# Optimization experiments

Measured on AMD Instinct MI355X. Metric: run time of the kernel, lower is better.

## Reference

```python
import jax, jax.numpy as jnp
import numpy as np

N = 50000      # num_nodes
NT = 300000    # unique (s, o) pairs
R = 64         # num relations
RP = 16        # latent pseudo-relations
E = 32         # emb_dim
C = 32         # num_classes
LW = 64        # latent MLP width


def setup_inputs() -> dict:
    key = jax.random.key(0)
    ks = jax.random.split(key, 12)
    inp = {
        "s_idx": jax.random.randint(ks[0], (NT,), 0, N, dtype=jnp.int32),
        "o_idx": jax.random.randint(ks[1], (NT,), 0, N, dtype=jnp.int32),
        "nhots": jax.random.uniform(ks[2], (NT, R), dtype=jnp.float32),
        "W1a": jax.random.normal(ks[3], (R, LW), dtype=jnp.float32) * 0.1,
        "b1a": jnp.zeros((LW,), jnp.float32),
        "W1b": jax.random.normal(ks[4], (LW, RP), dtype=jnp.float32) * 0.1,
        "b1b": jnp.zeros((RP,), jnp.float32),
        "W2a": jax.random.normal(ks[5], (R, LW), dtype=jnp.float32) * 0.1,
        "b2a": jnp.zeros((LW,), jnp.float32),
        "W2b": jax.random.normal(ks[6], (LW, RP), dtype=jnp.float32) * 0.1,
        "b2b": jnp.zeros((RP,), jnp.float32),
        "weights1": jax.random.normal(ks[7], (RP, N, E), dtype=jnp.float32) * 0.05,
        "weights2": jax.random.normal(ks[8], (RP, E, C), dtype=jnp.float32) * 0.05,
        "bias1": jnp.zeros((E,), jnp.float32),
        "bias2": jnp.zeros((C,), jnp.float32),
    }
    return inp


def _mlp(x, Wa, ba, Wb, bb):
    # Linear(r, lwidth) -> ReLU -> Linear(lwidth, rp)
    return jax.nn.relu(x @ Wa + ba) @ Wb + bb


def reference(s_idx, o_idx, nhots, W1a, b1a, W1b, b1b, W2a, b2a, W2b, b2b,
              weights1, weights2, bias1, bias2):
    n, rp = N, RP
    e = weights1.shape[2]
    k = jnp.arange(rp, dtype=s_idx.dtype)[:, None]   # [rp, 1]

    # hindices: rows = s (tiled k-major), cols = o * k  -> sparse (n, n*rp)
    hrows = jnp.tile(s_idx, rp)                       # [rp*nt]
    hcols = (o_idx[None, :] * k).reshape(-1)          # [rp*nt]
    # vindices: rows = s * k, cols = o (tiled)        -> sparse (n*rp, n)
    vrows = (s_idx[None, :] * k).reshape(-1)
    vcols = jnp.tile(o_idx, rp)

    # ---- layer 1: latent relation softmax + column-normalized spmm ----
    lat1 = jax.nn.softmax(_mlp(nhots, W1a, b1a, W1b, b1b), axis=1)  # [nt, rp]
    v1 = lat1.T.reshape(-1)                                          # [rp*nt], k-major
    colsum = jax.ops.segment_sum(v1, hcols, num_segments=n * rp)
    v1 = v1 / colsum[hcols]
    # spmm: out[s] += v1 * weights1.view(rp*n, e)[o*k]
    h = jax.ops.segment_sum(v1[:, None] * weights1.reshape(rp * n, e)[hcols],
                            hrows, num_segments=n)                   # [n, e]
    h = jax.nn.relu(h + bias1)

    # ---- layer 2: latent relation softmax + row-normalized spmm ----
    lat2 = jax.nn.softmax(_mlp(nhots, W2a, b2a, W2b, b2b), axis=1)   # [nt, rp]
    v2 = lat2.T.reshape(-1)
    rowsum = jax.ops.segment_sum(v2, vrows, num_segments=n * rp)
    v2 = v2 / rowsum[vrows]
    # spmm: out[s*k] += v2 * h[o]
    h2 = jax.ops.segment_sum(v2[:, None] * h[vcols],
                             vrows, num_segments=n * rp)             # [n*rp, e]
    h2 = h2.reshape(rp, n, e)

    out = jnp.einsum('rhc,rnh->nc', weights2, h2) + bias2            # [n, c]
    return out
```

## Files before the change

### kernel.cpp

```cpp
#include <hip/hip_runtime.h>
#include <hip/hip_bf16.h>

#define DEV_INLINE __device__ __forceinline__

constexpr int kN   = 50000;
constexpr int kNT  = 300000;
constexpr int kR   = 64;
constexpr int kRP  = 16;
constexpr int kE   = 32;
constexpr int kC   = 32;
constexpr int kLW  = 64;
constexpr int kNRP = kN * kRP;
constexpr int kChunks = (kN + 255) / 256;

typedef __attribute__((ext_vector_type(8))) short s8v;
typedef __attribute__((ext_vector_type(4))) float f32x4;

DEV_INLINE short f2bf(float f) {
  union { float f; unsigned u; } v; v.f = f;
  unsigned r = (v.u + 0x7fffu + ((v.u >> 16) & 1u)) >> 16;
  return (short)r;
}
DEV_INLINE float bf2f(short s) {
  union { unsigned u; float f; } v; v.u = ((unsigned)(unsigned short)s) << 16;
  return v.f;
}
DEV_INLINE float bflo(unsigned u) { union { unsigned x; float f; } a; a.x = u << 16;        return a.f; }
DEV_INLINE float bfhi(unsigned u) { union { unsigned x; float f; } a; a.x = u & 0xffff0000u; return a.f; }

__global__ void __launch_bounds__(256)
k_count(const int* __restrict__ s_idx, const int* __restrict__ o_idx,
        int* __restrict__ cnt_s, int* __restrict__ cnt_o) {
  const int e = blockIdx.x * 256 + threadIdx.x;
  if (e < kNT) {
    atomicAdd(&cnt_s[s_idx[e]], 1);
    atomicAdd(&cnt_o[o_idx[e]], 1);
  }
}

__global__ void __launch_bounds__(256)
k_scan_p1(const int* __restrict__ cnt_s, const int* __restrict__ cnt_o,
          int* __restrict__ rp_s, int* __restrict__ rp_o,
          int* __restrict__ bs_s, int* __restrict__ bs_o) {
  const int b = blockIdx.x;
  const bool iso = b >= kChunks;
  const int chunk = iso ? b - kChunks : b;
  const int* cnt = iso ? cnt_o : cnt_s;
  int* rp = iso ? rp_o : rp_s;
  int* bs = iso ? bs_o : bs_s;
  __shared__ int ws[4];
  const int tid = threadIdx.x, wave = tid >> 6, lane = tid & 63;
  const int i = chunk * 256 + tid;
  int v = (i < kN) ? cnt[i] : 0;
  int incl = v;
#pragma unroll
  for (int off = 1; off < 64; off <<= 1) {
    int tmp = __shfl_up(incl, off, 64);
    if (lane >= off) incl += tmp;
  }
  if (lane == 63) ws[wave] = incl;
  __syncthreads();
  int add = 0;
#pragma unroll
  for (int w = 0; w < 4; w++) if (w < wave) add += ws[w];
  incl += add;
  if (i < kN) rp[i + 1] = incl;
  if (tid == 255) bs[chunk] = incl;
}

__global__ void __launch_bounds__(256)
k_scan_p2(int* __restrict__ bs_s, int* __restrict__ bs_o) {
  __shared__ int ws[4];
  const int tid = threadIdx.x, wave = tid >> 6, lane = tid & 63;
#pragma unroll 1
  for (int a = 0; a < 2; a++) {
    int* bs = a ? bs_o : bs_s;
    const int v = (tid < kChunks) ? bs[tid] : 0;
    int incl = v;
#pragma unroll
    for (int off = 1; off < 64; off <<= 1) {
      int tmp = __shfl_up(incl, off, 64);
      if (lane >= off) incl += tmp;
    }
    if (lane == 63) ws[wave] = incl;
    __syncthreads();
    int add = 0;
#pragma unroll
    for (int w = 0; w < 4; w++) if (w < wave) add += ws[w];
    incl += add;
    __syncthreads();
    if (tid < kChunks) bs[tid] = incl - v;
    __syncthreads();
  }
}

__global__ void __launch_bounds__(256)
k_scan_p3(const int* __restrict__ bs_s, const int* __restrict__ bs_o,
          int* __restrict__ rp_s, int* __restrict__ rp_o) {
  const int b = blockIdx.x;
  const bool iso = b >= kChunks;
  const int chunk = iso ? b - kChunks : b;
  int* rp = iso ? rp_o : rp_s;
  const int* bs = iso ? bs_o : bs_s;
  const int i = chunk * 256 + threadIdx.x;
  if (i < kN) rp[i + 1] += bs[chunk];
  if (chunk == 0 && threadIdx.x == 0) rp[0] = 0;
}

__global__ void __launch_bounds__(256)
k_scatter2(const int* __restrict__ s_idx, const int* __restrict__ o_idx,
           const int* __restrict__ rowptr_s, int* __restrict__ cursor_s,
           const int* __restrict__ rowptr_o, int* __restrict__ cursor_o,
           int2* __restrict__ eo_s, int* __restrict__ e_o) {
  const int e = blockIdx.x * 256 + threadIdx.x;
  if (e < kNT) {
    const int s = s_idx[e], o = o_idx[e];
    const int ps = atomicAdd(&cursor_s[s], 1);
    int2 v; v.x = e; v.y = o;
    eo_s[rowptr_s[s] + ps] = v;
    const int po = atomicAdd(&cursor_o[o], 1);
    e_o[rowptr_o[o] + po] = e;
  }
}

__global__ void __launch_bounds__(256)
k_lat(const float* __restrict__ nhots,
      const float* __restrict__ W1a, const float* __restrict__ b1a,
      const float* __restrict__ W1b, const float* __restrict__ b1b,
      const float* __restrict__ W2a, const float* __restrict__ b2a,
      const float* __restrict__ W2b, const float* __restrict__ b2b,
      float* __restrict__ lat1o, float* __restrict__ lat2o) {
  __shared__ float sWa[2][kR * kLW];
  __shared__ float sWb[2][kLW * kRP];
  __shared__ float sb[2][kLW + kRP];
  __shared__ float sHf[4][32][68];
  const int tid = threadIdx.x;
  const int wave = tid >> 6, lane = tid & 63;
  const int p = lane & 15, q = lane >> 4, q8 = (lane >> 4) * 8;

  for (int i = tid; i < kR * kLW; i += 256) { sWa[0][i] = W1a[i]; sWa[1][i] = W2a[i]; }
  for (int i = tid; i < kLW * kRP; i += 256) { sWb[0][i] = W1b[i]; sWb[1][i] = W2b[i]; }
  if (tid < kLW) { sb[0][tid] = b1a[tid]; sb[1][tid] = b2a[tid]; }
  else if (tid < kLW + kRP) { sb[0][tid] = b1b[tid - kLW]; sb[1][tid] = b2b[tid - kLW]; }
  __syncthreads();

  const int w2 = (blockIdx.x * 4 + wave) * 2;

#pragma unroll 1
  for (int mlp = 0; mlp < 2; mlp++) {
    s8v Bh[4][2], Bl[4][2], Bbh[2], Bbl[2];
    float bav[4];
#pragma unroll
    for (int nt = 0; nt < 4; nt++) {
#pragma unroll
      for (int ks = 0; ks < 2; ks++)
#pragma unroll
        for (int j = 0; j < 8; j++) {
          const float v = sWa[mlp][(ks * 32 + q8 + j) * kLW + nt * 16 + p];
          const short h = f2bf(v);
          Bh[nt][ks][j] = h;
          Bl[nt][ks][j] = f2bf(v - bf2f(h));
        }
      bav[nt] = sb[mlp][nt * 16 + p];
    }
#pragma unroll
    for (int ks = 0; ks < 2; ks++)
#pragma unroll
      for (int j = 0; j < 8; j++) {
        const float v = sWb[mlp][(ks * 32 + q8 + j) * kRP + p];
        const short h = f2bf(v);
        Bbh[ks][j] = h;
        Bbl[ks][j] = f2bf(v - bf2f(h));
      }
    const float bbv = sb[mlp][kLW + p];
    float* lato = mlp ? lat2o : lat1o;

#pragma unroll 1
    for (int t = 0; t < 2; t++) {
      const int slot = w2 + t;
      if (slot >= kNT / 32) break;
      const int eb = slot * 32;
#pragma unroll
      for (int ht = 0; ht < 2; ht++) {
        const int mb = eb + ht * 16;
        const float* arow = nhots + (size_t)(mb + p) * kR;
        s8v ah[2], al[2];
#pragma unroll
        for (int ks = 0; ks < 2; ks++) {
          const float4 xa = *(const float4*)(arow + ks * 32 + q8);
          const float4 xb = *(const float4*)(arow + ks * 32 + q8 + 4);
          const float fv[8] = {xa.x, xa.y, xa.z, xa.w, xb.x, xb.y, xb.z, xb.w};
#pragma unroll
          for (int j = 0; j < 8; j++) {
            const short h = f2bf(fv[j]);
            ah[ks][j] = h;
            al[ks][j] = f2bf(fv[j] - bf2f(h));
          }
        }
        f32x4 acc[4];
#pragma unroll
        for (int nt = 0; nt < 4; nt++) {
          acc[nt] = (f32x4)0.f;
#pragma unroll
          for (int ks = 0; ks < 2; ks++) {
            acc[nt] = __builtin_amdgcn_mfma_f32_16x16x32_bf16(ah[ks], Bh[nt][ks], acc[nt], 0, 0, 0);
            acc[nt] = __builtin_amdgcn_mfma_f32_16x16x32_bf16(ah[ks], Bl[nt][ks], acc[nt], 0, 0, 0);
            acc[nt] = __builtin_amdgcn_mfma_f32_16x16x32_bf16(al[ks], Bh[nt][ks], acc[nt], 0, 0, 0);
          }
        }
#pragma unroll
        for (int nt = 0; nt < 4; nt++)
#pragma unroll
          for (int reg = 0; reg < 4; reg++)
            sHf[wave][ht * 16 + q * 4 + reg][nt * 16 + p] = fmaxf(acc[nt][reg] + bav[nt], 0.f);
      }
#pragma unroll
      for (int ht = 0; ht < 2; ht++) {
        const int mb = eb + ht * 16;
        const float* hr = &sHf[wave][ht * 16 + p][0];
        s8v ah[2], al[2];
#pragma unroll
        for (int ks = 0; ks < 2; ks++) {
          const float4 xa = *(const float4*)(hr + ks * 32 + q8);
          const float4 xb = *(const float4*)(hr + ks * 32 + q8 + 4);
          const float fv[8] = {xa.x, xa.y, xa.z, xa.w, xb.x, xb.y, xb.z, xb.w};
#pragma unroll
          for (int j = 0; j < 8; j++) {
            const short h = f2bf(fv[j]);
            ah[ks][j] = h;
            al[ks][j] = f2bf(fv[j] - bf2f(h));
          }
        }
        f32x4 acc = (f32x4)0.f;
#pragma unroll
        for (int ks = 0; ks < 2; ks++) {
          acc = __builtin_amdgcn_mfma_f32_16x16x32_bf16(ah[ks], Bbh[ks], acc, 0, 0, 0);
          acc = __builtin_amdgcn_mfma_f32_16x16x32_bf16(ah[ks], Bbl[ks], acc, 0, 0, 0);
          acc = __builtin_amdgcn_mfma_f32_16x16x32_bf16(al[ks], Bbh[ks], acc, 0, 0, 0);
        }
#pragma unroll
        for (int reg = 0; reg < 4; reg++) {
          const float v = acc[reg] + bbv;
          float m = v;
#pragma unroll
          for (int d = 1; d < 16; d <<= 1) m = fmaxf(m, __shfl_xor(m, d));
          const float e = __expf(v - m);
          float sum = e;
#pragma unroll
          for (int d = 1; d < 16; d <<= 1) sum += __shfl_xor(sum, d);
          lato[(size_t)(mb + q * 4 + reg) * kRP + p] = e / sum;
        }
      }
    }
  }
}

__global__ void __launch_bounds__(256)
k_partials(const int* __restrict__ rowptr_s, const int2* __restrict__ eo_s,
           const int* __restrict__ rowptr_o, const int* __restrict__ e_o,
           const float* __restrict__ lat1, const float* __restrict__ lat2,
           float* __restrict__ C1, float* __restrict__ R2,
           float* __restrict__ tots) {
  __shared__ float st[2][4];
  const int tid = threadIdx.x;
  const int wave = tid >> 6, lane = tid & 63;
  const int k = lane & 15, g = lane >> 4;
  float t1 = 0.f, t2 = 0.f;
  const int nw = gridDim.x * 4;
  for (int n = blockIdx.x * 4 + wave; n < kN; n += nw) {
    {
      const int beg = rowptr_s[n], end = rowptr_s[n + 1];
      float acc = 0.f;
      for (int j = beg + g; j < end; j += 4)
        acc += lat2[(size_t)eo_s[j].x * kRP + k];
      acc += __shfl_xor(acc, 16); acc += __shfl_xor(acc, 32);
      if (g == 0) { R2[n * kRP + k] = acc; if (k == 0) t2 += acc; }
    }
    {
      const int beg = rowptr_o[n], end = rowptr_o[n + 1];
      float acc = 0.f;
      for (int j = beg + g; j < end; j += 4)
        acc += lat1[(size_t)e_o[j] * kRP + k];
      acc += __shfl_xor(acc, 16); acc += __shfl_xor(acc, 32);
      if (g == 0) { C1[n * kRP + k] = acc; if (k == 0) t1 += acc; }
    }
  }
  if (lane == 0) { st[0][wave] = t1; st[1][wave] = t2; }
  __syncthreads();
  if (tid == 0) {
    atomicAdd(&tots[0], st[0][0] + st[0][1] + st[0][2] + st[0][3]);
    atomicAdd(&tots[1], st[1][0] + st[1][1] + st[1][2] + st[1][3]);
  }
}

__global__ void __launch_bounds__(256)
k_norms(const float* __restrict__ C1, const float* __restrict__ R2,
        const float* __restrict__ tots,
        float* __restrict__ csinv, float* __restrict__ rsinv) {
  const int m = blockIdx.x * 256 + threadIdx.x;
  if (m < kNRP) {
    float cs = (m == 0) ? tots[0] : 0.f;
    float rs = (m == 0) ? tots[1] : 0.f;
#pragma unroll
    for (int k = 1; k < kRP; k++) {
      if (m % k == 0) {
        const int q = m / k;
        if (q < kN) { cs += C1[q * kRP + k]; rs += R2[q * kRP + k]; }
      }
    }
    csinv[m] = (cs != 0.f) ? 1.f / cs : 0.f;
    rsinv[m] = (rs != 0.f) ? 1.f / rs : 0.f;
  }
}

__global__ void __launch_bounds__(256)
k_gbuild(const float* __restrict__ wt1, const float* __restrict__ csinv,
         unsigned* __restrict__ G8u) {
  __shared__ float sT[16][33];
  const int o = blockIdx.x;
  const int tid = threadIdx.x;
#pragma unroll
  for (int half = 0; half < 2; half++) {
    const int e = half * 256 + tid;
    const int k = e >> 5, c = e & 31;
    const int idx = o * k;
    sT[k][c] = csinv[idx] * wt1[(size_t)idx * kE + c];
  }
  __syncthreads();
  const int l = tid >> 2;
  const int c = l >> 1, kh = l & 1;
  const int j0 = (2 * tid) & 7;
  const int k0 = kh * 8 + j0, k1 = k0 + 1;
  const unsigned lo = (unsigned short)f2bf(sT[k0][c]);
  const unsigned hi = (unsigned short)f2bf(sT[k1][c]);
  G8u[(size_t)o * 256 + tid] = lo | (hi << 16);
}

__global__ void __launch_bounds__(256)
k_layer1g(const int* __restrict__ rowptr, const int2* __restrict__ eo,
          const float* __restrict__ lat1, const uint4* __restrict__ G8,
          const float* __restrict__ bias1, float* __restrict__ h) {
  const int tid = threadIdx.x;
  const int wave = tid >> 6, lane = tid & 63;
  const int c = lane >> 1, kh = lane & 1;
  const float b1 = bias1[c];
  for (int s = blockIdx.x * 4 + wave; s < kN; s += gridDim.x * 4) {
    float acc = 0.f;
    const int beg = rowptr[s], end = rowptr[s + 1];
    for (int j = beg; j < end; j++) {
      const int2 E = eo[j];
      const uint4 g = G8[(size_t)E.y * 64 + lane];
      const float4 la = *(const float4*)(lat1 + (size_t)E.x * kRP + kh * 8);
      const float4 lb = *(const float4*)(lat1 + (size_t)E.x * kRP + kh * 8 + 4);
      acc = fmaf(la.x, bflo(g.x), acc); acc = fmaf(la.y, bfhi(g.x), acc);
      acc = fmaf(la.z, bflo(g.y), acc); acc = fmaf(la.w, bfhi(g.y), acc);
      acc = fmaf(lb.x, bflo(g.z), acc); acc = fmaf(lb.y, bfhi(g.z), acc);
      acc = fmaf(lb.z, bflo(g.w), acc); acc = fmaf(lb.w, bfhi(g.w), acc);
    }
    acc += __shfl_xor(acc, 1);
    if (kh == 0) h[(size_t)s * kE + c] = fmaxf(acc + b1, 0.f);
  }
}

__global__ void __launch_bounds__(256)
k_u(const int* __restrict__ rowptr, const int2* __restrict__ eo,
    const float* __restrict__ lat2, const float* __restrict__ rsinv,
    const float* __restrict__ h, short* __restrict__ Ub,
    float* __restrict__ pblk) {
  __shared__ float sacc[kE];
  const int tid = threadIdx.x;
  const int wave = tid >> 6, lane = tid & 63;
  const int c = lane & 31, half = lane >> 5;
  if (tid < kE) sacc[tid] = 0.f;
  __syncthreads();
  float hpart = 0.f;
  for (int s = blockIdx.x * 4 + wave; s < kN; s += gridDim.x * 4) {
    float u[8];
#pragma unroll
    for (int kk = 0; kk < 8; kk++) u[kk] = 0.f;
    const int beg = rowptr[s], end = rowptr[s + 1];
    for (int j = beg; j < end; j++) {
      const int2 E = eo[j];
      const float hv = h[(size_t)E.y * kE + c];
      const float4* lp = (const float4*)(lat2 + (size_t)E.x * kRP) + half * 2;
      const float4 la = lp[0], lb = lp[1];
      const float lv[8] = {la.x, la.y, la.z, la.w, lb.x, lb.y, lb.z, lb.w};
#pragma unroll
      for (int kk = 0; kk < 8; kk++) u[kk] = fmaf(lv[kk], hv, u[kk]);
    }
    if (half == 0) hpart += u[0];
#pragma unroll
    for (int kk = 0; kk < 8; kk++) {
      const int k = half * 8 + kk;
      if (k >= 1)
        Ub[((size_t)s * 15 + (k - 1)) * kE + c] = f2bf(u[kk] * rsinv[s * k]);
    }
  }
  atomicAdd(&sacc[c], hpart);
  __syncthreads();
  if (tid < kE) pblk[(size_t)blockIdx.x * kE + tid] = sacc[tid];
}

__global__ void __launch_bounds__(256)
k_hred(const float* __restrict__ pblk, int nblk, float* __restrict__ hrow0) {
  __shared__ float sacc[kE];
  const int tid = threadIdx.x;
  if (tid < kE) sacc[tid] = 0.f;
  __syncthreads();
  const int total = nblk * kE;
  float r = 0.f;
  for (int i = blockIdx.x * 256 + tid; i < total; i += gridDim.x * 256)
    r += pblk[i];
  atomicAdd(&sacc[tid & 31], r);
  __syncthreads();
  if (tid < kE) atomicAdd(&hrow0[tid], sacc[tid]);
}

__global__ void __launch_bounds__(256)
k_h2(const short* __restrict__ Ub, const float* __restrict__ hrow0,
     const float* __restrict__ rsinv, short* __restrict__ H2) {
  const int tid = threadIdx.x;
  const int g = tid >> 5, c = tid & 31;
  const int n = blockIdx.x * 8 + g;
  const float rs0 = rsinv[0];
#pragma unroll 1
  for (int r = 0; r < kRP; r++) {
    const int m = r * kN + n;
    float row = (m == 0) ? hrow0[c] * rs0 : 0.f;
#pragma unroll
    for (int k = 1; k < kRP; k++) {
      if (m % k == 0) {
        const int s = m / k;
        if (s < kN) row += bf2f(Ub[((size_t)s * 15 + (k - 1)) * kE + c]);
      }
    }
    H2[((size_t)n * kRP + r) * kE + c] = f2bf(row);
  }
}

__global__ void __launch_bounds__(256)
k_einsum(const short* __restrict__ H2, const float* __restrict__ W2,
         const float* __restrict__ bias2, float* __restrict__ out) {
  __shared__ short sBWh[16 * 2 * 64 * 8];
  __shared__ short sBWl[16 * 2 * 64 * 8];
  const int tid = threadIdx.x;
  for (int i = tid; i < 16384; i += 256) {
    const int j = i & 7, ln = (i >> 3) & 63, nt = (i >> 9) & 1, ks = i >> 10;
    const int pp = ln & 15, qq8 = (ln >> 4) * 8;
    const float v = W2[(ks * 32 + qq8 + j) * 32 + nt * 16 + pp];
    const short h = f2bf(v);
    sBWh[i] = h;
    sBWl[i] = f2bf(v - bf2f(h));
  }
  __syncthreads();
  const int wave = tid >> 6, lane = tid & 63;
  const int p = lane & 15, q = lane >> 4, q8 = q * 8;
  const float bias0 = bias2[p], bias1v = bias2[16 + p];
  for (int tile = blockIdx.x * 4 + wave; tile < kN / 16; tile += gridDim.x * 4) {
    const int mb = tile * 16;
    f32x4 acc0 = (f32x4)0.f, acc1 = (f32x4)0.f;
    const short* arow = H2 + (size_t)(mb + p) * 512 + q8;
#pragma unroll
    for (int ks = 0; ks < 16; ks++) {
      const s8v a   = *(const s8v*)(arow + ks * 32);
      const s8v b0h = *(const s8v*)(sBWh + ((ks * 2 + 0) * 64 + lane) * 8);
      const s8v b0l = *(const s8v*)(sBWl + ((ks * 2 + 0) * 64 + lane) * 8);
      const s8v b1h = *(const s8v*)(sBWh + ((ks * 2 + 1) * 64 + lane) * 8);
      const s8v b1l = *(const s8v*)(sBWl + ((ks * 2 + 1) * 64 + lane) * 8);
      acc0 = __builtin_amdgcn_mfma_f32_16x16x32_bf16(a, b0h, acc0, 0, 0, 0);
      acc0 = __builtin_amdgcn_mfma_f32_16x16x32_bf16(a, b0l, acc0, 0, 0, 0);
      acc1 = __builtin_amdgcn_mfma_f32_16x16x32_bf16(a, b1h, acc1, 0, 0, 0);
      acc1 = __builtin_amdgcn_mfma_f32_16x16x32_bf16(a, b1l, acc1, 0, 0, 0);
    }
#pragma unroll
    for (int reg = 0; reg < 4; reg++) {
      const int n = mb + q * 4 + reg;
      out[(size_t)n * kC + p]      = acc0[reg] + bias0;
      out[(size_t)n * kC + 16 + p] = acc1[reg] + bias1v;
    }
  }
}

extern "C" void kernel_launch(void* const* d_in, const int* in_sizes, int n_in,
                              void* d_out, int out_size, void* d_ws, size_t ws_size,
                              hipStream_t stream) {
  (void)in_sizes; (void)n_in; (void)out_size; (void)ws_size;
  const int* s_idx = (const int*)d_in[0];
  const int* o_idx = (const int*)d_in[1];
  const float* nhots = (const float*)d_in[2];
  const float* W1a = (const float*)d_in[3]; const float* b1a = (const float*)d_in[4];
  const float* W1b = (const float*)d_in[5]; const float* b1b = (const float*)d_in[6];
  const float* W2a = (const float*)d_in[7]; const float* b2a = (const float*)d_in[8];
  const float* W2b = (const float*)d_in[9]; const float* b2b = (const float*)d_in[10];
  const float* wt1 = (const float*)d_in[11]; const float* wt2 = (const float*)d_in[12];
  const float* bias1 = (const float*)d_in[13]; const float* bias2 = (const float*)d_in[14];

  char* ws = (char*)d_ws;
  size_t off = 0;
  auto alloc = [&](size_t bytes) -> char* {
    char* p = ws + off;
    off = (off + bytes + 255) & ~(size_t)255;
    return p;
  };
  char*  z0       = ws;
  int*   cnt_s    = (int*)  alloc((size_t)kN * 4);
  int*   cnt_o    = (int*)  alloc((size_t)kN * 4);
  int*   cursor_s = (int*)  alloc((size_t)kN * 4);
  int*   cursor_o = (int*)  alloc((size_t)kN * 4);
  float* tots     = (float*)alloc(8);
  float* hrow0    = (float*)alloc((size_t)kE * 4);
  const size_t zbytes = (size_t)((ws + off) - z0);
  int*   bs_s     = (int*)  alloc((size_t)kChunks * 4);
  int*   bs_o     = (int*)  alloc((size_t)kChunks * 4);
  int*   rowptr_s = (int*)  alloc((size_t)(kN + 1) * 4);
  int*   rowptr_o = (int*)  alloc((size_t)(kN + 1) * 4);
  float* pblk     = (float*)alloc((size_t)12500 * kE * 4);
  float* lat2     = (float*)alloc((size_t)kNT * kRP * 4);
  int2*  eo_s     = (int2*) alloc((size_t)kNT * 8);
  int*   e_o      = (int*)  alloc((size_t)kNT * 4);
  float* C1       = (float*)alloc((size_t)kNRP * 4);
  float* R2       = (float*)alloc((size_t)kNRP * 4);
  float* csinv    = (float*)alloc((size_t)kNRP * 4);
  float* rsinv    = (float*)alloc((size_t)kNRP * 4);
  float* hbuf     = (float*)alloc((size_t)kN * kE * 4);
  short* Ub       = (short*)alloc((size_t)kN * 15 * kE * 2);
  char*  Greg     = alloc((size_t)kN * 1024);
  float* lat1     = (float*)Ub;
  unsigned* G8u   = (unsigned*)Greg;
  short* H2       = (short*)Greg;

  hipMemsetAsync(z0, 0, zbytes, stream);

  const dim3 blk(256);
  const int gEdges = (kNT + 255) / 256;
  const int gLat = ((kNT / 32 + 1) / 2 + 3) / 4;

  k_count<<<gEdges, blk, 0, stream>>>(s_idx, o_idx, cnt_s, cnt_o);
  k_scan_p1<<<2 * kChunks, blk, 0, stream>>>(cnt_s, cnt_o, rowptr_s, rowptr_o, bs_s, bs_o);
  k_scan_p2<<<1, blk, 0, stream>>>(bs_s, bs_o);
  k_scan_p3<<<2 * kChunks, blk, 0, stream>>>(bs_s, bs_o, rowptr_s, rowptr_o);
  k_scatter2<<<gEdges, blk, 0, stream>>>(s_idx, o_idx, rowptr_s, cursor_s,
                                         rowptr_o, cursor_o, eo_s, e_o);
  k_lat<<<gLat, blk, 0, stream>>>(nhots, W1a, b1a, W1b, b1b,
                                  W2a, b2a, W2b, b2b, lat1, lat2);
  k_partials<<<512, blk, 0, stream>>>(rowptr_s, eo_s, rowptr_o, e_o,
                                      lat1, lat2, C1, R2, tots);
  k_norms<<<(kNRP + 255) / 256, blk, 0, stream>>>(C1, R2, tots, csinv, rsinv);
  k_gbuild<<<kN, blk, 0, stream>>>(wt1, csinv, G8u);
  k_layer1g<<<12500, blk, 0, stream>>>(rowptr_s, eo_s, lat1, (const uint4*)G8u, bias1, hbuf);
  k_u<<<12500, blk, 0, stream>>>(rowptr_s, eo_s, lat2, rsinv, hbuf, Ub, pblk);
  k_hred<<<50, blk, 0, stream>>>(pblk, 12500, hrow0);
  k_h2<<<kN / 8, blk, 0, stream>>>(Ub, hrow0, rsinv, H2);
  k_einsum<<<782, blk, 0, stream>>>(H2, wt2, bias2, (float*)d_out);
}
```

Baseline: 685.6 us.

## Precompute MFMA weight fragments once, fuse lat MLP stages, simplify H2 divisibility

Adds a single-block kernel that converts the MLP weights into bf16 hi/lo MFMA fragment layout once, so each k_lat block loads fragments directly instead of staging fp32 weights in shared memory and splitting them. The two MLP stages in k_lat are fused per 16-row half, which shrinks the shared buffer and uses a truncation-based hi/lo split. k_h2 replaces per-element modulo/division tests with precomputed n%k residues and fully unrolled r loops. This trades one extra launch and changed hi-part rounding (truncation instead of round-to-nearest) for lower per-block setup and less integer work.

```diff
diff --git a/kernel.cpp b/kernel.cpp
--- a/kernel.cpp
+++ b/kernel.cpp
@@ -27,6 +27,30 @@
 }
 DEV_INLINE float bflo(unsigned u) { union { unsigned x; float f; } a; a.x = u << 16;        return a.f; }
 DEV_INLINE float bfhi(unsigned u) { union { unsigned x; float f; } a; a.x = u & 0xffff0000u; return a.f; }
+
+union U4S8 { uint4 u; s8v s; };
+
+DEV_INLINE void split8(const float4 A, const float4 B, s8v& hi, s8v& lo) {
+  const float f[8] = {A.x, A.y, A.z, A.w, B.x, B.y, B.z, B.w};
+  unsigned u[8], l[8];
+#pragma unroll
+  for (int i = 0; i < 8; i++) { union { float f; unsigned u; } c; c.f = f[i]; u[i] = c.u; }
+#pragma unroll
+  for (int i = 0; i < 8; i++) {
+    union { unsigned u; float f; } t; t.u = u[i] & 0xffff0000u;
+    union { float f; unsigned u; } c; c.f = f[i] - t.f; l[i] = c.u;
+  }
+  U4S8 H, L;
+  H.u.x = (u[1] & 0xffff0000u) | (u[0] >> 16);
+  H.u.y = (u[3] & 0xffff0000u) | (u[2] >> 16);
+  H.u.z = (u[5] & 0xffff0000u) | (u[4] >> 16);
+  H.u.w = (u[7] & 0xffff0000u) | (u[6] >> 16);
+  L.u.x = (l[1] & 0xffff0000u) | (l[0] >> 16);
+  L.u.y = (l[3] & 0xffff0000u) | (l[2] >> 16);
+  L.u.z = (l[5] & 0xffff0000u) | (l[4] >> 16);
+  L.u.w = (l[7] & 0xffff0000u) | (l[6] >> 16);
+  hi = H.s; lo = L.s;
+}
 
 __global__ void __launch_bounds__(256)
 k_count(const int* __restrict__ s_idx, const int* __restrict__ o_idx,
@@ -124,55 +148,75 @@
 }
 
 __global__ void __launch_bounds__(256)
-k_lat(const float* __restrict__ nhots,
-      const float* __restrict__ W1a, const float* __restrict__ b1a,
-      const float* __restrict__ W1b, const float* __restrict__ b1b,
-      const float* __restrict__ W2a, const float* __restrict__ b2a,
-      const float* __restrict__ W2b, const float* __restrict__ b2b,
+k_wprep(const float* __restrict__ W1a, const float* __restrict__ W1b,
+        const float* __restrict__ W2a, const float* __restrict__ W2b,
+        short* __restrict__ Wf) {
+  const int tid = threadIdx.x;
+  for (int i = tid; i < 8192; i += 256) {
+    const int j = i & 7, lane = (i >> 3) & 63, ks = (i >> 9) & 1,
+              nt = (i >> 10) & 3, mlp = i >> 12;
+    const int p = lane & 15, q8 = (lane >> 4) * 8;
+    const float* Wa = mlp ? W2a : W1a;
+    const float v = Wa[(ks * 32 + q8 + j) * kLW + nt * 16 + p];
+    union { float f; unsigned u; } c; c.f = v;
+    const short h = (short)(c.u >> 16);
+    Wf[i] = h;
+    Wf[8192 + i] = f2bf(v - bf2f(h));
+  }
+  for (int i = tid; i < 2048; i += 256) {
+    const int j = i & 7, lane = (i >> 3) & 63, ks = (i >> 9) & 1, mlp = i >> 10;
+    const int p = lane & 15, q8 = (lane >> 4) * 8;
+    const float* Wb = mlp ? W2b : W1b;
+    const float v = Wb[(ks * 32 + q8 + j) * kRP + p];
+    union { float f; unsigned u; } c; c.f = v;
+    const short h = (short)(c.u >> 16);
+    Wf[16384 + i] = h;
+    Wf[18432 + i] = f2bf(v - bf2f(h));
+  }
+}
+
+__global__ void __launch_bounds__(256)
+k_lat(const float* __restrict__ nhots, const short* __restrict__ Wf,
+      const float* __restrict__ b1a, const float* __restrict__ b1b,
+      const float* __restrict__ b2a, const float* __restrict__ b2b,
       float* __restrict__ lat1o, float* __restrict__ lat2o) {
-  __shared__ float sWa[2][kR * kLW];
-  __shared__ float sWb[2][kLW * kRP];
-  __shared__ float sb[2][kLW + kRP];
-  __shared__ float sHf[4][32][68];
+  __shared__ float sHf[4][16][68];
   const int tid = threadIdx.x;
   const int wave = tid >> 6, lane = tid & 63;
   const int p = lane & 15, q = lane >> 4, q8 = (lane >> 4) * 8;
 
-  for (int i = tid; i < kR * kLW; i += 256) { sWa[0][i] = W1a[i]; sWa[1][i] = W2a[i]; }
-  for (int i = tid; i < kLW * kRP; i += 256) { sWb[0][i] = W1b[i]; sWb[1][i] = W2b[i]; }
-  if (tid < kLW) { sb[0][tid] = b1a[tid]; sb[1][tid] = b2a[tid]; }
-  else if (tid < kLW + kRP) { sb[0][tid] = b1b[tid - kLW]; sb[1][tid] = b2b[tid - kLW]; }
-  __syncthreads();
+  const uint4* BaH4 = (const uint4*)(Wf);
+  const uint4* BaL4 = (const uint4*)(Wf + 8192);
+  const uint4* BbH4 = (const uint4*)(Wf + 16384);
+  const uint4* BbL4 = (const uint4*)(Wf + 18432);
 
   const int w2 = (blockIdx.x * 4 + wave) * 2;
 
 #pragma unroll 1
   for (int mlp = 0; mlp < 2; mlp++) {
     s8v Bh[4][2], Bl[4][2], Bbh[2], Bbl[2];
+#pragma unroll
+    for (int nt = 0; nt < 4; nt++)
+#pragma unroll
+      for (int ks = 0; ks < 2; ks++) {
+        U4S8 a, b;
+        a.u = BaH4[((mlp * 4 + nt) * 2 + ks) * 64 + lane];
+        b.u = BaL4[((mlp * 4 + nt) * 2 + ks) * 64 + lane];
+        Bh[nt][ks] = a.s; Bl[nt][ks] = b.s;
+      }
+#pragma unroll
+    for (int ks = 0; ks < 2; ks++) {
+      U4S8 a, b;
+      a.u = BbH4[(mlp * 2 + ks) * 64 + lane];
+      b.u = BbL4[(mlp * 2 + ks) * 64 + lane];
+      Bbh[ks] = a.s; Bbl[ks] = b.s;
+    }
+    const float* bA = mlp ? b2a : b1a;
+    const float* bB = mlp ? b2b : b1b;
     float bav[4];
 #pragma unroll
-    for (int nt = 0; nt < 4; nt++) {
-#pragma unroll
-      for (int ks = 0; ks < 2; ks++)
-#pragma unroll
-        for (int j = 0; j < 8; j++) {
-          const float v = sWa[mlp][(ks * 32 + q8 + j) * kLW + nt * 16 + p];
-          const short h = f2bf(v);
-          Bh[nt][ks][j] = h;
-          Bl[nt][ks][j] = f2bf(v - bf2f(h));
-        }
-      bav[nt] = sb[mlp][nt * 16 + p];
-    }
-#pragma unroll
-    for (int ks = 0; ks < 2; ks++)
-#pragma unroll
-      for (int j = 0; j < 8; j++) {
-        const float v = sWb[mlp][(ks * 32 + q8 + j) * kRP + p];
-        const short h = f2bf(v);
-        Bbh[ks][j] = h;
-        Bbl[ks][j] = f2bf(v - bf2f(h));
-      }
-    const float bbv = sb[mlp][kLW + p];
+    for (int nt = 0; nt < 4; nt++) bav[nt] = bA[nt * 16 + p];
+    const float bbv = bB[p];
     float* lato = mlp ? lat2o : lat1o;
 
 #pragma unroll 1
@@ -180,7 +224,7 @@
       const int slot = w2 + t;
       if (slot >= kNT / 32) break;
       const int eb = slot * 32;
-#pragma unroll
+#pragma unroll 1
       for (int ht = 0; ht < 2; ht++) {
         const int mb = eb + ht * 16;
         const float* arow = nhots + (size_t)(mb + p) * kR;
@@ -189,13 +233,7 @@
         for (int ks = 0; ks < 2; ks++) {
           const float4 xa = *(const float4*)(arow + ks * 32 + q8);
           const float4 xb = *(const float4*)(arow + ks * 32 + q8 + 4);
-          const float fv[8] = {xa.x, xa.y, xa.z, xa.w, xb.x, xb.y, xb.z, xb.w};
-#pragma unroll
-          for (int j = 0; j < 8; j++) {
-            const short h = f2bf(fv[j]);
-            ah[ks][j] = h;
-            al[ks][j] = f2bf(fv[j] - bf2f(h));
-          }
+          split8(xa, xb, ah[ks], al[ks]);
         }
         f32x4 acc[4];
 #pragma unroll
@@ -212,35 +250,25 @@
         for (int nt = 0; nt < 4; nt++)
 #pragma unroll
           for (int reg = 0; reg < 4; reg++)
-            sHf[wave][ht * 16 + q * 4 + reg][nt * 16 + p] = fmaxf(acc[nt][reg] + bav[nt], 0.f);
-      }
-#pragma unroll
-      for (int ht = 0; ht < 2; ht++) {
-        const int mb = eb + ht * 16;
-        const float* hr = &sHf[wave][ht * 16 + p][0];
-        s8v ah[2], al[2];
+            sHf[wave][q * 4 + reg][nt * 16 + p] = fmaxf(acc[nt][reg] + bav[nt], 0.f);
+        const float* hr = &sHf[wave][p][0];
+        s8v hh[2], hl[2];
 #pragma unroll
         for (int ks = 0; ks < 2; ks++) {
           const float4 xa = *(const float4*)(hr + ks * 32 + q8);
           const float4 xb = *(const float4*)(hr + ks * 32 + q8 + 4);
-          const float fv[8] = {xa.x, xa.y, xa.z, xa.w, xb.x, xb.y, xb.z, xb.w};
-#pragma unroll
-          for (int j = 0; j < 8; j++) {
-            const short h = f2bf(fv[j]);
-            ah[ks][j] = h;
-            al[ks][j] = f2bf(fv[j] - bf2f(h));
-          }
+          split8(xa, xb, hh[ks], hl[ks]);
         }
-        f32x4 acc = (f32x4)0.f;
+        f32x4 accB = (f32x4)0.f;
 #pragma unroll
         for (int ks = 0; ks < 2; ks++) {
-          acc = __builtin_amdgcn_mfma_f32_16x16x32_bf16(ah[ks], Bbh[ks], acc, 0, 0, 0);
-          acc = __builtin_amdgcn_mfma_f32_16x16x32_bf16(ah[ks], Bbl[ks], acc, 0, 0, 0);
-          acc = __builtin_amdgcn_mfma_f32_16x16x32_bf16(al[ks], Bbh[ks], acc, 0, 0, 0);
+          accB = __builtin_amdgcn_mfma_f32_16x16x32_bf16(hh[ks], Bbh[ks], accB, 0, 0, 0);
+          accB = __builtin_amdgcn_mfma_f32_16x16x32_bf16(hh[ks], Bbl[ks], accB, 0, 0, 0);
+          accB = __builtin_amdgcn_mfma_f32_16x16x32_bf16(hl[ks], Bbh[ks], accB, 0, 0, 0);
         }
 #pragma unroll
         for (int reg = 0; reg < 4; reg++) {
-          const float v = acc[reg] + bbv;
+          const float v = accB[reg] + bbv;
           float m = v;
 #pragma unroll
           for (int d = 1; d < 16; d <<= 1) m = fmaxf(m, __shfl_xor(m, d));
@@ -423,15 +451,20 @@
   const int g = tid >> 5, c = tid & 31;
   const int n = blockIdx.x * 8 + g;
   const float rs0 = rsinv[0];
-#pragma unroll 1
+  int nm[16];
+  nm[0] = 0; nm[1] = 0;
+#pragma unroll
+  for (int k = 2; k < kRP; k++) nm[k] = n % k;
+#pragma unroll
   for (int r = 0; r < kRP; r++) {
-    const int m = r * kN + n;
-    float row = (m == 0) ? hrow0[c] * rs0 : 0.f;
-#pragma unroll
-    for (int k = 1; k < kRP; k++) {
-      if (m % k == 0) {
-        const int s = m / k;
-        if (s < kN) row += bf2f(Ub[((size_t)s * 15 + (k - 1)) * kE + c]);
+    float row = 0.f;
+    if (r == 0 && n == 0) row = hrow0[c] * rs0;
+#pragma unroll
+    for (int k = r + 1; k < kRP; k++) {
+      const int target = (k - (r * 50000) % k) % k;
+      if (nm[k] == target) {
+        const int s = (r * 50000 + n) / k;
+        row += bf2f(Ub[((size_t)s * 15 + (k - 1)) * kE + c]);
       }
     }
     H2[((size_t)n * kRP + r) * kE + c] = f2bf(row);
@@ -510,6 +543,7 @@
   float* tots     = (float*)alloc(8);
   float* hrow0    = (float*)alloc((size_t)kE * 4);
   const size_t zbytes = (size_t)((ws + off) - z0);
+  short* Wf       = (short*)alloc((size_t)20480 * 2);
   int*   bs_s     = (int*)  alloc((size_t)kChunks * 4);
   int*   bs_o     = (int*)  alloc((size_t)kChunks * 4);
   int*   rowptr_s = (int*)  alloc((size_t)(kN + 1) * 4);
@@ -541,8 +575,8 @@
   k_scan_p3<<<2 * kChunks, blk, 0, stream>>>(bs_s, bs_o, rowptr_s, rowptr_o);
   k_scatter2<<<gEdges, blk, 0, stream>>>(s_idx, o_idx, rowptr_s, cursor_s,
                                          rowptr_o, cursor_o, eo_s, e_o);
-  k_lat<<<gLat, blk, 0, stream>>>(nhots, W1a, b1a, W1b, b1b,
-                                  W2a, b2a, W2b, b2b, lat1, lat2);
+  k_wprep<<<1, blk, 0, stream>>>(W1a, W1b, W2a, W2b, Wf);
+  k_lat<<<gLat, blk, 0, stream>>>(nhots, Wf, b1a, b1b, b2a, b2b, lat1, lat2);
   k_partials<<<512, blk, 0, stream>>>(rowptr_s, eo_s, rowptr_o, e_o,
                                       lat1, lat2, C1, R2, tots);
   k_norms<<<(kNRP + 255) / 256, blk, 0, stream>>>(C1, R2, tots, csinv, rsinv);
```

New measurement: 642.9 us. 6.2% less time.
